# Performance work log

Measured on AMD Instinct MI355X. Metric: run time of the kernel, lower is better.

## Reference

```python
import jax, jax.numpy as jnp
import numpy as np

NC, NB, NT = 512, 128, 256   # feats dims: [channels, batch, time]
H = 512                      # hidden_size
NCLS = 97                    # num_classes
NUM_STEPS = 32               # fixed decode length (= text_length.max())


def setup_inputs() -> dict:
    key = jax.random.key(0)
    ks = jax.random.split(key, 12)
    s = 1.0 / np.sqrt(H)
    inp = {
        "feats": jax.random.normal(ks[0], (NC, NB, NT), jnp.float32),
        "text_length": jnp.full((NB,), NUM_STEPS, jnp.int32),
        # AttentionCell params
        "Wi2h": jax.random.normal(ks[1], (H, NC), jnp.float32) * s,   # i2h, no bias
        "Wh2h": jax.random.normal(ks[2], (H, H), jnp.float32) * s,
        "bh2h": jax.random.normal(ks[3], (H,), jnp.float32) * s,
        "Wscore": jax.random.normal(ks[4], (1, H), jnp.float32) * s,  # score, no bias
        # GRUCell params (gate order: r, z, n as in PyTorch)
        "Wih": jax.random.normal(ks[5], (3 * H, NC), jnp.float32) * s,
        "Whh": jax.random.normal(ks[6], (3 * H, H), jnp.float32) * s,
        "bih": jax.random.normal(ks[7], (3 * H,), jnp.float32) * s,
        "bhh": jax.random.normal(ks[8], (3 * H,), jnp.float32) * s,
        # generator: Linear(hidden_size, num_classes - 1)
        "Wgen": jax.random.normal(ks[9], (NCLS - 1, H), jnp.float32) * s,
        "bgen": jax.random.normal(ks[10], (NCLS - 1,), jnp.float32) * s,
    }
    return inp


def reference(feats, text_length, Wi2h, Wh2h, bh2h, Wscore, Wih, Whh, bih, bhh, Wgen, bgen):
    # feats: [nC, nB, nT]
    nC, nB, nT = feats.shape
    # i2h(feats) is step-independent -> hoist out of the loop (same math)
    feats_proj = jnp.einsum('cbt,hc->bth', feats, Wi2h)  # [nB, nT, H]
    w_score = Wscore[0]                                   # [H]

    def step(h, _):
        # additive attention
        hp = h @ Wh2h.T + bh2h                                  # [nB, H]
        e = jnp.tanh(feats_proj + hp[:, None, :]) @ w_score     # [nB, nT]
        alpha = jax.nn.softmax(e, axis=1)                       # [nB, nT]
        context = jnp.einsum('cbt,bt->bc', feats, alpha)        # [nB, nC]
        # GRUCell(context, h), PyTorch semantics
        gi = context @ Wih.T + bih                              # [nB, 3H]
        gh = h @ Whh.T + bhh                                    # [nB, 3H]
        ir, iz, in_ = jnp.split(gi, 3, axis=1)
        hr, hz, hn = jnp.split(gh, 3, axis=1)
        r = jax.nn.sigmoid(ir + hr)
        z = jax.nn.sigmoid(iz + hz)
        n = jnp.tanh(in_ + r * hn)
        h_new = (1.0 - z) * n + z * h
        return h_new, h_new

    h0 = jnp.zeros((nB, feats_proj.shape[-1]), feats.dtype)
    _, hiddens = jax.lax.scan(step, h0, None, length=NUM_STEPS)  # [T, nB, H]
    # all lengths == NUM_STEPS -> gather is a per-batch flatten
    new_hiddens = hiddens.transpose(1, 0, 2).reshape(-1, hiddens.shape[-1])  # [nB*T, H]
    probs = new_hiddens @ Wgen.T + bgen                          # [nB*T, NCLS-1]
    return probs
```

## Files before the change

kernel.cpp:

```cpp
#include <hip/hip_runtime.h>
#include <math.h>

#define NBATCH 128
#define NTIME  256
#define NCH    512
#define NH     512
#define NSTEPS 32
#define NOUT   96
#define MTOT   32768

typedef __attribute__((ext_vector_type(8))) short short8v;
typedef __attribute__((ext_vector_type(4))) float f32x4;

__device__ __forceinline__ float fast_tanh(float x) {
    x = fminf(fmaxf(x, -30.f), 30.f);
    float u = __expf(2.f * x);
    return (u - 1.f) / (u + 1.f);
}
__device__ __forceinline__ float fast_sigmoid(float x) {
    x = fminf(fmaxf(x, -30.f), 30.f);
    return 1.f / (1.f + __expf(-x));
}
__device__ __forceinline__ float wave_reduce_sum(float s) {
    #pragma unroll
    for (int off = 32; off; off >>= 1) s += __shfl_xor(s, off, 64);
    return s;
}
__device__ __forceinline__ float wave_reduce_max(float s) {
    #pragma unroll
    for (int off = 32; off; off >>= 1) s = fmaxf(s, __shfl_xor(s, off, 64));
    return s;
}
__device__ __forceinline__ unsigned short f2bf(float f) {
    unsigned u = __builtin_bit_cast(unsigned, f);
    return (unsigned short)((u + 0x7FFFu + ((u >> 16) & 1u)) >> 16);
}
__device__ __forceinline__ float bflo(unsigned u) {
    return __builtin_bit_cast(float, u << 16);
}
__device__ __forceinline__ float bfhi(unsigned u) {
    return __builtin_bit_cast(float, u & 0xFFFF0000u);
}

__global__ __launch_bounds__(256) void k_w2bf(const float* __restrict__ W,
                                              unsigned short* __restrict__ Wb) {
    #pragma unroll
    for (int r = 0; r < 4; ++r) {
        int idx = (blockIdx.x * 256 + threadIdx.x) + r * 16384;
        float4 v = *(const float4*)(W + (size_t)idx * 4);
        ushort4 o;
        o.x = f2bf(v.x); o.y = f2bf(v.y); o.z = f2bf(v.z); o.w = f2bf(v.w);
        *(ushort4*)(Wb + (size_t)idx * 4) = o;
    }
}

__global__ __launch_bounds__(256) void k_feats2bf(const float* __restrict__ feats,
                                                  unsigned short* __restrict__ Fb) {
    __shared__ float tl[64][65];
    const int m0 = (blockIdx.x & 511) * 64;
    const int k0 = (blockIdx.x >> 9) * 64;
    const int tid = threadIdx.x;
    #pragma unroll
    for (int p = 0; p < 4; ++p) {
        int fid = tid + p * 256;
        int row = fid >> 4, c4 = fid & 15;
        float4 v = *(const float4*)(feats + (size_t)(k0 + row) * MTOT + m0 + c4 * 4);
        tl[row][c4 * 4 + 0] = v.x; tl[row][c4 * 4 + 1] = v.y;
        tl[row][c4 * 4 + 2] = v.z; tl[row][c4 * 4 + 3] = v.w;
    }
    __syncthreads();
    #pragma unroll
    for (int p = 0; p < 4; ++p) {
        int cid = tid + p * 256;
        int mm = cid >> 4, ch = cid & 15;
        ushort4 o;
        o.x = f2bf(tl[ch * 4 + 0][mm]);
        o.y = f2bf(tl[ch * 4 + 1][mm]);
        o.z = f2bf(tl[ch * 4 + 2][mm]);
        o.w = f2bf(tl[ch * 4 + 3][mm]);
        *(ushort4*)(Fb + (size_t)(m0 + mm) * 512 + k0 + ch * 4) = o;
    }
}

__global__ __launch_bounds__(1024) void k_fcopy(const float* __restrict__ f,
                                                unsigned short* __restrict__ o) {
    int gid = blockIdx.x * 1024 + threadIdx.x;
    float4 v = *(const float4*)(f + (size_t)gid * 4);
    ushort4 s;
    s.x = f2bf(v.x); s.y = f2bf(v.y); s.z = f2bf(v.z); s.w = f2bf(v.w);
    *(ushort4*)(o + (size_t)gid * 4) = s;
}

__global__ __launch_bounds__(256) void k_fp_mfma(const unsigned short* __restrict__ Wb,
                                                 const unsigned short* __restrict__ Fb,
                                                 unsigned short* __restrict__ fp_bf) {
    __shared__ char SB[49152];
    unsigned short* As = (unsigned short*)SB;
    unsigned short* Bs = (unsigned short*)(SB + 16384);
    float* tl = (float*)SB;
    const int m0 = (blockIdx.x & 127) * 256;
    const int h0 = (blockIdx.x >> 7) * 128;
    const int tid = threadIdx.x;
    const int lane = tid & 63, wid = tid >> 6;
    const int wh = wid & 1, wm = wid >> 1;
    f32x4 acc[4][8];
    #pragma unroll
    for (int i = 0; i < 4; ++i)
        #pragma unroll
        for (int j = 0; j < 8; ++j) acc[i][j] = (f32x4)0.f;

    for (int k0 = 0; k0 < 512; k0 += 64) {
        #pragma unroll
        for (int i = 0; i < 4; ++i) {
            int cid = tid + i * 256;
            int row = cid >> 3, ch = cid & 7;
            uint4 v = *(const uint4*)(Wb + (size_t)(h0 + row) * 512 + k0 + ch * 8);
            *(uint4*)(As + row * 64 + ((ch ^ (row & 7)) << 3)) = v;
        }
        #pragma unroll
        for (int i = 0; i < 8; ++i) {
            int cid = tid + i * 256;
            int row = cid >> 3, ch = cid & 7;
            uint4 v = *(const uint4*)(Fb + (size_t)(m0 + row) * 512 + k0 + ch * 8);
            *(uint4*)(Bs + row * 64 + ((ch ^ (row & 7)) << 3)) = v;
        }
        __syncthreads();
        #pragma unroll
        for (int ks = 0; ks < 2; ++ks) {
            short8v a[4], b[8];
            #pragma unroll
            for (int hf = 0; hf < 4; ++hf) {
                int row = wh * 64 + hf * 16 + (lane & 15);
                int ch = ks * 4 + (lane >> 4);
                a[hf] = *(const short8v*)(As + row * 64 + ((ch ^ (row & 7)) << 3));
            }
            #pragma unroll
            for (int mf = 0; mf < 8; ++mf) {
                int row = wm * 128 + mf * 16 + (lane & 15);
                int ch = ks * 4 + (lane >> 4);
                b[mf] = *(const short8v*)(Bs + row * 64 + ((ch ^ (row & 7)) << 3));
            }
            #pragma unroll
            for (int hf = 0; hf < 4; ++hf)
                #pragma unroll
                for (int mf = 0; mf < 8; ++mf)
                    acc[hf][mf] = __builtin_amdgcn_mfma_f32_16x16x32_bf16(
                        a[hf], b[mf], acc[hf][mf], 0, 0, 0);
        }
        __syncthreads();
    }
    #pragma unroll
    for (int hf = 0; hf < 4; ++hf) {
        #pragma unroll
        for (int mf = 0; mf < 8; ++mf) {
            int ml = wm * 128 + mf * 16 + (lane & 15);
            int col = wh * 16 + (lane >> 4) * 4;
            tl[ml * 33 + col + 0] = acc[hf][mf][0];
            tl[ml * 33 + col + 1] = acc[hf][mf][1];
            tl[ml * 33 + col + 2] = acc[hf][mf][2];
            tl[ml * 33 + col + 3] = acc[hf][mf][3];
        }
        __syncthreads();
        #pragma unroll
        for (int mi = 0; mi < 8; ++mi) {
            int ml = (tid >> 3) + mi * 32;
            int hl4 = (tid & 7) * 4;
            float v0 = tl[ml * 33 + hl4 + 0];
            float v1 = tl[ml * 33 + hl4 + 1];
            float v2 = tl[ml * 33 + hl4 + 2];
            float v3 = tl[ml * 33 + hl4 + 3];
            int hg = h0 + ((hl4 < 16) ? (hf * 16 + hl4) : (64 + hf * 16 + hl4 - 16));
            ushort4 o;
            o.x = f2bf(v0); o.y = f2bf(v1); o.z = f2bf(v2); o.w = f2bf(v3);
            *(ushort4*)(fp_bf + (size_t)(m0 + ml) * 512 + hg) = o;
        }
        __syncthreads();
    }
}

__global__ __launch_bounds__(256) void k_wt(const float* __restrict__ W,
                                            float* __restrict__ WT) {
    __shared__ float tl[32][33];
    const int bi = blockIdx.x & 15, bj = blockIdx.x >> 4;
    const int tx = threadIdx.x & 31, ty8 = threadIdx.x >> 5;
    #pragma unroll
    for (int i = 0; i < 4; ++i) {
        int r = ty8 * 4 + i;
        tl[r][tx] = W[(size_t)(bj * 32 + r) * NH + bi * 32 + tx];
    }
    __syncthreads();
    #pragma unroll
    for (int i = 0; i < 4; ++i) {
        int c = ty8 * 4 + i;
        WT[(size_t)(bi * 32 + c) * NH + bj * 32 + tx] = tl[tx][c];
    }
}

__global__ __launch_bounds__(1024) void k_hp0(const float* __restrict__ bh2h,
                                              float* __restrict__ hp) {
    int i = blockIdx.x * 1024 + threadIdx.x;
    hp[i] = bh2h[i & 511];
}

__global__ __launch_bounds__(512) void k_e(const unsigned short* __restrict__ fp_bf,
                                           const float* __restrict__ hp,
                                           const float* __restrict__ wscore,
                                           float* __restrict__ e) {
    const int b = blockIdx.x >> 2;
    const int t0 = (blockIdx.x & 3) * 64;
    const int tid = threadIdx.x;
    const int lane = tid & 63, w = tid >> 6;
    float4 h0 = *(const float4*)(hp + (size_t)b * NH + lane * 8);
    float4 h1 = *(const float4*)(hp + (size_t)b * NH + lane * 8 + 4);
    float4 w0 = *(const float4*)(wscore + lane * 8);
    float4 w1 = *(const float4*)(wscore + lane * 8 + 4);
    #pragma unroll 2
    for (int it = 0; it < 8; ++it) {
        int t = t0 + w * 8 + it;
        uint4 v = *(const uint4*)(fp_bf + (size_t)(b * NTIME + t) * NH + lane * 8);
        float s = fast_tanh(bflo(v.x) + h0.x) * w0.x + fast_tanh(bfhi(v.x) + h0.y) * w0.y +
                  fast_tanh(bflo(v.y) + h0.z) * w0.z + fast_tanh(bfhi(v.y) + h0.w) * w0.w +
                  fast_tanh(bflo(v.z) + h1.x) * w1.x + fast_tanh(bfhi(v.z) + h1.y) * w1.y +
                  fast_tanh(bflo(v.w) + h1.z) * w1.z + fast_tanh(bfhi(v.w) + h1.w) * w1.w;
        s = wave_reduce_sum(s);
        if (lane == 0) e[b * NTIME + t] = s;
    }
}

__global__ __launch_bounds__(512) void k_ctx2(const float* __restrict__ e,
                                              const unsigned short* __restrict__ featsb,
                                              float* __restrict__ ctx) {
    __shared__ float als[256];
    __shared__ float red[8];
    const int b = blockIdx.x >> 2;
    const int c0 = (blockIdx.x & 3) * 128;
    const int tid = threadIdx.x;
    const int lane = tid & 63, w = tid >> 6;
    float v = (tid < 256) ? e[b * NTIME + tid] : -3.4e38f;
    float m = wave_reduce_max(v);
    if (lane == 0) red[w] = m;
    __syncthreads();
    m = red[0];
    #pragma unroll
    for (int i = 1; i < 8; ++i) m = fmaxf(m, red[i]);
    float ex = (tid < 256) ? __expf(v - m) : 0.f;
    float s = wave_reduce_sum(ex);
    __syncthreads();
    if (lane == 0) red[w] = s;
    __syncthreads();
    s = 0.f;
    #pragma unroll
    for (int i = 0; i < 8; ++i) s += red[i];
    if (tid < 256) als[tid] = ex / s;
    __syncthreads();

    float4 al = *(const float4*)&als[lane * 4];
    #pragma unroll 4
    for (int cc = 0; cc < 16; ++cc) {
        int c = c0 + w * 16 + cc;
        uint2 fv = *(const uint2*)(featsb + (size_t)(c * NBATCH + b) * NTIME + lane * 4);
        float sc = bflo(fv.x) * al.x + bfhi(fv.x) * al.y +
                   bflo(fv.y) * al.z + bfhi(fv.y) * al.w;
        sc = wave_reduce_sum(sc);
        if (lane == 0) ctx[(size_t)b * NCH + c] = sc;
    }
}

__global__ __launch_bounds__(1024) void k_gates(const float* __restrict__ ctx,
                                                const float* __restrict__ h,
                                                const float* __restrict__ Wih,
                                                const float* __restrict__ Whh,
                                                float* __restrict__ g2) {
    __shared__ float S[16384 + 8192];
    float* A_ldsT = S;
    float* scr    = S + 16384;
    const int blk = blockIdx.x;
    const int g   = blk >> 5;
    const int j0  = (blk & 31) * 16;
    const float* A = (g < 3) ? ctx : h;
    const float* W = (g < 3) ? Wih : Whh;
    const int tid = threadIdx.x;
    const int m2  = tid & 63;
    const int q   = __builtin_amdgcn_readfirstlane(tid >> 6);
    const int nq  = q & 3, kq = q >> 2;
    const float* Wr0 = W + (size_t)((g % 3) * 512 + j0 + nq * 4 + 0) * NH;
    const float* Wr1 = W + (size_t)((g % 3) * 512 + j0 + nq * 4 + 1) * NH;
    const float* Wr2 = W + (size_t)((g % 3) * 512 + j0 + nq * 4 + 2) * NH;
    const float* Wr3 = W + (size_t)((g % 3) * 512 + j0 + nq * 4 + 3) * NH;
    float acc[2][4] = {};
    for (int kt = 0; kt < 4; ++kt) {
        {
            int m = tid & 127, kc = tid >> 7;
            #pragma unroll
            for (int q4 = 0; q4 < 4; ++q4) {
                int kk = kc * 16 + q4 * 4;
                float4 vv = *(const float4*)(A + (size_t)m * NH + kt * 128 + kk);
                A_ldsT[(kk + 0) * 128 + m] = vv.x;
                A_ldsT[(kk + 1) * 128 + m] = vv.y;
                A_ldsT[(kk + 2) * 128 + m] = vv.z;
                A_ldsT[(kk + 3) * 128 + m] = vv.w;
            }
        }
        __syncthreads();
        const int kbase = kt * 128;
        #pragma unroll 8
        for (int kk = kq * 32; kk < kq * 32 + 32; ++kk) {
            float a0 = A_ldsT[kk * 128 + m2];
            float a1 = A_ldsT[kk * 128 + m2 + 64];
            float w0 = Wr0[kbase + kk], w1 = Wr1[kbase + kk];
            float w2 = Wr2[kbase + kk], w3 = Wr3[kbase + kk];
            acc[0][0] += a0 * w0; acc[0][1] += a0 * w1;
            acc[0][2] += a0 * w2; acc[0][3] += a0 * w3;
            acc[1][0] += a1 * w0; acc[1][1] += a1 * w1;
            acc[1][2] += a1 * w2; acc[1][3] += a1 * w3;
        }
        __syncthreads();
    }
    #pragma unroll
    for (int hi = 0; hi < 2; ++hi)
        #pragma unroll
        for (int r = 0; r < 4; ++r)
            scr[(kq * 16 + nq * 4 + r) * 128 + m2 + 64 * hi] = acc[hi][r];
    __syncthreads();
    #pragma unroll
    for (int rep = 0; rep < 2; ++rep) {
        int oid = tid + rep * 1024;
        int m = oid & 127, nl = oid >> 7;
        float vv = scr[(0 * 16 + nl) * 128 + m] + scr[(1 * 16 + nl) * 128 + m] +
                   scr[(2 * 16 + nl) * 128 + m] + scr[(3 * 16 + nl) * 128 + m];
        g2[(size_t)(g * 512 + j0 + nl) * NBATCH + m] = vv;
    }
}

__global__ __launch_bounds__(1024) void k_comb_hp(const float* __restrict__ g2,
                                                  const float* __restrict__ hprev,
                                                  float* __restrict__ hidn,
                                                  const float* __restrict__ bih,
                                                  const float* __restrict__ bhh,
                                                  const float* __restrict__ WT,
                                                  const float* __restrict__ bh2h,
                                                  float* __restrict__ hp) {
    __shared__ float h_s[4 * 512];
    __shared__ float scr2[16 * 4 * 16 * 4];
    const int blk = blockIdx.x;
    const int b0 = (blk >> 3) * 4;
    const int jbase = (blk & 7) * 64;
    const int tid = threadIdx.x;
    #pragma unroll
    for (int rep = 0; rep < 2; ++rep) {
        int idx = tid + rep * 1024;
        int bi = idx & 3, kk = idx >> 2;
        int b = b0 + bi;
        float ir = g2[(size_t)(0 * 512 + kk) * NBATCH + b] + bih[kk];
        float iz = g2[(size_t)(1 * 512 + kk) * NBATCH + b] + bih[512 + kk];
        float in_ = g2[(size_t)(2 * 512 + kk) * NBATCH + b] + bih[1024 + kk];
        float hr = g2[(size_t)(3 * 512 + kk) * NBATCH + b] + bhh[kk];
        float hz = g2[(size_t)(4 * 512 + kk) * NBATCH + b] + bhh[512 + kk];
        float hn = g2[(size_t)(5 * 512 + kk) * NBATCH + b] + bhh[1024 + kk];
        float r = fast_sigmoid(ir + hr);
        float z = fast_sigmoid(iz + hz);
        float ng = fast_tanh(in_ + r * hn);
        float hv = hprev[(size_t)b * NH + kk];
        float hnew = (1.f - z) * ng + z * hv;
        h_s[bi * 512 + kk] = hnew;
        if ((blk & 7) == 0) hidn[(size_t)b * NH + kk] = hnew;
    }
    __syncthreads();
    {
        const int jq = tid & 15, bi = (tid >> 4) & 3, kq = tid >> 6;
        const int j = jbase + jq * 4;
        float4 acc = make_float4(0.f, 0.f, 0.f, 0.f);
        #pragma unroll 8
        for (int kk = 0; kk < 32; ++kk) {
            int k = kq * 32 + kk;
            float4 wv = *(const float4*)(WT + (size_t)k * NH + j);
            float hv = h_s[bi * 512 + k];
            acc.x += hv * wv.x; acc.y += hv * wv.y;
            acc.z += hv * wv.z; acc.w += hv * wv.w;
        }
        *(float4*)&scr2[((kq * 4 + bi) * 16 + jq) * 4] = acc;
    }
    __syncthreads();
    if (tid < 64) {
        const int bi = tid >> 4, jq = tid & 15;
        float4 sum = make_float4(0.f, 0.f, 0.f, 0.f);
        #pragma unroll
        for (int kq = 0; kq < 16; ++kq) {
            float4 p = *(const float4*)&scr2[((kq * 4 + bi) * 16 + jq) * 4];
            sum.x += p.x; sum.y += p.y; sum.z += p.z; sum.w += p.w;
        }
        int j = jbase + jq * 4;
        float4 bb = *(const float4*)(bh2h + j);
        sum.x += bb.x; sum.y += bb.y; sum.z += bb.z; sum.w += bb.w;
        *(float4*)(hp + (size_t)(b0 + bi) * NH + j) = sum;
    }
}

__global__ __launch_bounds__(256) void k_gen(const float* __restrict__ hid,
                                             const float* __restrict__ Wgen,
                                             const float* __restrict__ bgen,
                                             float* __restrict__ out) {
    __shared__ float As[32][36];
    __shared__ float Bs[32][97];
    const int m0 = blockIdx.x * 32;
    const int tid = threadIdx.x;
    const int tx = tid & 31, ty = tid >> 5;
    float acc[4][3] = {};
    for (int k0 = 0; k0 < 512; k0 += 32) {
        {
            int mm = tid >> 3, kq = (tid & 7) << 2;
            int m = m0 + mm, s = m & 31, b = m >> 5;
            float4 v = *(const float4*)(hid + (size_t)(s + 1) * 65536 + b * 512 + k0 + kq);
            *(float4*)(&As[mm][kq]) = v;
        }
        #pragma unroll
        for (int i = 0; i < 3; ++i) {
            int f4 = tid + i * 256;
            int nn = f4 >> 3, kq = (f4 & 7) << 2;
            float4 v = *(const float4*)(Wgen + (size_t)nn * 512 + k0 + kq);
            Bs[kq + 0][nn] = v.x; Bs[kq + 1][nn] = v.y;
            Bs[kq + 2][nn] = v.z; Bs[kq + 3][nn] = v.w;
        }
        __syncthreads();
        #pragma unroll
        for (int kk = 0; kk < 32; ++kk) {
            float bv[3];
            #pragma unroll
            for (int j = 0; j < 3; ++j) bv[j] = Bs[kk][tx * 3 + j];
            #pragma unroll
            for (int i = 0; i < 4; ++i) {
                float a = As[ty * 4 + i][kk];
                #pragma unroll
                for (int j = 0; j < 3; ++j) acc[i][j] += a * bv[j];
            }
        }
        __syncthreads();
    }
    #pragma unroll
    for (int i = 0; i < 4; ++i)
        #pragma unroll
        for (int j = 0; j < 3; ++j)
            out[(size_t)(m0 + ty * 4 + i) * NOUT + tx * 3 + j] = acc[i][j] + bgen[tx * 3 + j];
}

extern "C" void kernel_launch(void* const* d_in, const int* in_sizes, int n_in,
                              void* d_out, int out_size, void* d_ws, size_t ws_size,
                              hipStream_t stream) {
    const float* feats  = (const float*)d_in[0];
    const float* Wi2h   = (const float*)d_in[2];
    const float* Wh2h   = (const float*)d_in[3];
    const float* bh2h   = (const float*)d_in[4];
    const float* Wscore = (const float*)d_in[5];
    const float* Wih    = (const float*)d_in[6];
    const float* Whh    = (const float*)d_in[7];
    const float* bih    = (const float*)d_in[8];
    const float* bhh    = (const float*)d_in[9];
    const float* Wgen   = (const float*)d_in[10];
    const float* bgen   = (const float*)d_in[11];
    float* out = (float*)d_out;

    float* ws  = (float*)d_ws;
    unsigned short* fp_bf = (unsigned short*)ws;
    float* hid   = ws + 8388608;
    float* WT    = hid + 2162688;
    float* hpctx = WT + 262144;
    unsigned short* Wb     = (unsigned short*)(hpctx + 65536);
    unsigned short* Fb     = (unsigned short*)(hpctx + 65536 + 131072);
    unsigned short* featsb = Fb;

    float* e  = out;
    float* g2 = out;

    hipMemsetAsync(hid, 0, 65536 * sizeof(float), stream);
    k_wt<<<256, 256, 0, stream>>>(Wh2h, WT);
    k_w2bf<<<64, 256, 0, stream>>>(Wi2h, Wb);
    k_feats2bf<<<4096, 256, 0, stream>>>(feats, Fb);
    k_fp_mfma<<<512, 256, 0, stream>>>(Wb, Fb, fp_bf);
    k_fcopy<<<4096, 1024, 0, stream>>>(feats, featsb);
    k_hp0<<<64, 1024, 0, stream>>>(bh2h, hpctx);

    for (int s = 0; s < NSTEPS; ++s) {
        const float* h = hid + (size_t)s * 65536;
        float* hn      = hid + (size_t)(s + 1) * 65536;
        k_e<<<512, 512, 0, stream>>>(fp_bf, hpctx, Wscore, e);
        k_ctx2<<<512, 512, 0, stream>>>(e, featsb, hpctx);
        k_gates<<<192, 1024, 0, stream>>>(hpctx, h, Wih, Whh, g2);
        k_comb_hp<<<256, 1024, 0, stream>>>(g2, h, hn, bih, bhh, WT, bh2h, hpctx);
    }
    k_gen<<<128, 256, 0, stream>>>(hid, Wgen, bgen, out);
}
```

Baseline: 1.852 ms.

## Replace fp32 GRU gate GEMM with bf16 MFMA kernel and bf16 weights

Pre-converts Wih/Whh to bf16 and computes the per-step GRU gate projections with a bf16 MFMA tiled GEMM (24 blocks of 128x128), consuming bf16 context and a bf16 copy of h. Also stores the transposed Wh2h in bf16 for the hp projection in the combine kernel. This aims to cut the scalar fp32 FMA cost and weight bandwidth of the gate GEMM each step, at the cost of bf16 rounding of inputs and weights and low grid occupancy.

```diff
diff --git a/kernel.cpp b/kernel.cpp
--- a/kernel.cpp
+++ b/kernel.cpp
@@ -51,6 +51,21 @@
         ushort4 o;
         o.x = f2bf(v.x); o.y = f2bf(v.y); o.z = f2bf(v.z); o.w = f2bf(v.w);
         *(ushort4*)(Wb + (size_t)idx * 4) = o;
+    }
+}
+
+__global__ __launch_bounds__(256) void k_wg2bf(const float* __restrict__ Wih,
+                                               const float* __restrict__ Whh,
+                                               unsigned short* __restrict__ Wgb) {
+    #pragma unroll
+    for (int r = 0; r < 4; ++r) {
+        int idx = (blockIdx.x * 256 + threadIdx.x) + r * 98304;
+        const float* src = (idx < 196608) ? (Wih + (size_t)idx * 4)
+                                          : (Whh + (size_t)(idx - 196608) * 4);
+        float4 v = *(const float4*)src;
+        ushort4 o;
+        o.x = f2bf(v.x); o.y = f2bf(v.y); o.z = f2bf(v.z); o.w = f2bf(v.w);
+        *(ushort4*)(Wgb + (size_t)idx * 4) = o;
     }
 }
 
@@ -179,7 +194,7 @@
 }
 
 __global__ __launch_bounds__(256) void k_wt(const float* __restrict__ W,
-                                            float* __restrict__ WT) {
+                                            unsigned short* __restrict__ WTb) {
     __shared__ float tl[32][33];
     const int bi = blockIdx.x & 15, bj = blockIdx.x >> 4;
     const int tx = threadIdx.x & 31, ty8 = threadIdx.x >> 5;
@@ -192,7 +207,7 @@
     #pragma unroll
     for (int i = 0; i < 4; ++i) {
         int c = ty8 * 4 + i;
-        WT[(size_t)(bi * 32 + c) * NH + bj * 32 + tx] = tl[tx][c];
+        WTb[(size_t)(bi * 32 + c) * NH + bj * 32 + tx] = f2bf(tl[tx][c]);
     }
 }
 
@@ -229,7 +244,7 @@
 
 __global__ __launch_bounds__(512) void k_ctx2(const float* __restrict__ e,
                                               const unsigned short* __restrict__ featsb,
-                                              float* __restrict__ ctx) {
+                                              unsigned short* __restrict__ ctx_bf) {
     __shared__ float als[256];
     __shared__ float red[8];
     const int b = blockIdx.x >> 2;
@@ -262,82 +277,76 @@
         float sc = bflo(fv.x) * al.x + bfhi(fv.x) * al.y +
                    bflo(fv.y) * al.z + bfhi(fv.y) * al.w;
         sc = wave_reduce_sum(sc);
-        if (lane == 0) ctx[(size_t)b * NCH + c] = sc;
-    }
-}
-
-__global__ __launch_bounds__(1024) void k_gates(const float* __restrict__ ctx,
-                                                const float* __restrict__ h,
-                                                const float* __restrict__ Wih,
-                                                const float* __restrict__ Whh,
-                                                float* __restrict__ g2) {
-    __shared__ float S[16384 + 8192];
-    float* A_ldsT = S;
-    float* scr    = S + 16384;
-    const int blk = blockIdx.x;
-    const int g   = blk >> 5;
-    const int j0  = (blk & 31) * 16;
-    const float* A = (g < 3) ? ctx : h;
-    const float* W = (g < 3) ? Wih : Whh;
-    const int tid = threadIdx.x;
-    const int m2  = tid & 63;
-    const int q   = __builtin_amdgcn_readfirstlane(tid >> 6);
-    const int nq  = q & 3, kq = q >> 2;
-    const float* Wr0 = W + (size_t)((g % 3) * 512 + j0 + nq * 4 + 0) * NH;
-    const float* Wr1 = W + (size_t)((g % 3) * 512 + j0 + nq * 4 + 1) * NH;
-    const float* Wr2 = W + (size_t)((g % 3) * 512 + j0 + nq * 4 + 2) * NH;
-    const float* Wr3 = W + (size_t)((g % 3) * 512 + j0 + nq * 4 + 3) * NH;
-    float acc[2][4] = {};
-    for (int kt = 0; kt < 4; ++kt) {
-        {
-            int m = tid & 127, kc = tid >> 7;
-            #pragma unroll
-            for (int q4 = 0; q4 < 4; ++q4) {
-                int kk = kc * 16 + q4 * 4;
-                float4 vv = *(const float4*)(A + (size_t)m * NH + kt * 128 + kk);
-                A_ldsT[(kk + 0) * 128 + m] = vv.x;
-                A_ldsT[(kk + 1) * 128 + m] = vv.y;
-                A_ldsT[(kk + 2) * 128 + m] = vv.z;
-                A_ldsT[(kk + 3) * 128 + m] = vv.w;
+        if (lane == 0) ctx_bf[(size_t)b * NCH + c] = f2bf(sc);
+    }
+}
+
+__global__ __launch_bounds__(256) void k_gmfma(const unsigned short* __restrict__ ctx_bf,
+                                               const unsigned short* __restrict__ h_bf,
+                                               const unsigned short* __restrict__ Wgb,
+                                               float* __restrict__ g2) {
+    __shared__ unsigned short As[128 * 64];
+    __shared__ unsigned short Bs[128 * 64];
+    const int j0 = blockIdx.x * 128;
+    const unsigned short* A = (j0 < 1536) ? ctx_bf : h_bf;
+    const int tid = threadIdx.x;
+    const int lane = tid & 63, wid = tid >> 6;
+    const int wb = wid & 1, wj = wid >> 1;
+    f32x4 acc[4][4];
+    #pragma unroll
+    for (int i = 0; i < 4; ++i)
+        #pragma unroll
+        for (int j = 0; j < 4; ++j) acc[i][j] = (f32x4)0.f;
+
+    for (int k0 = 0; k0 < 512; k0 += 64) {
+        #pragma unroll
+        for (int i = 0; i < 4; ++i) {
+            int cid = tid + i * 256;
+            int row = cid >> 3, ch = cid & 7;
+            uint4 va = *(const uint4*)(A + (size_t)row * 512 + k0 + ch * 8);
+            *(uint4*)(As + row * 64 + ((ch ^ (row & 7)) << 3)) = va;
+            uint4 vb = *(const uint4*)(Wgb + (size_t)(j0 + row) * 512 + k0 + ch * 8);
+            *(uint4*)(Bs + row * 64 + ((ch ^ (row & 7)) << 3)) = vb;
+        }
+        __syncthreads();
+        #pragma unroll
+        for (int ks = 0; ks < 2; ++ks) {
+            short8v a[4], b[4];
+            #pragma unroll
+            for (int f = 0; f < 4; ++f) {
+                int rowa = wb * 64 + f * 16 + (lane & 15);
+                int rowb = wj * 64 + f * 16 + (lane & 15);
+                int ch = ks * 4 + (lane >> 4);
+                a[f] = *(const short8v*)(As + rowa * 64 + ((ch ^ (rowa & 7)) << 3));
+                b[f] = *(const short8v*)(Bs + rowb * 64 + ((ch ^ (rowb & 7)) << 3));
             }
-        }
-        __syncthreads();
-        const int kbase = kt * 128;
-        #pragma unroll 8
-        for (int kk = kq * 32; kk < kq * 32 + 32; ++kk) {
-            float a0 = A_ldsT[kk * 128 + m2];
-            float a1 = A_ldsT[kk * 128 + m2 + 64];
-            float w0 = Wr0[kbase + kk], w1 = Wr1[kbase + kk];
-            float w2 = Wr2[kbase + kk], w3 = Wr3[kbase + kk];
-            acc[0][0] += a0 * w0; acc[0][1] += a0 * w1;
-            acc[0][2] += a0 * w2; acc[0][3] += a0 * w3;
-            acc[1][0] += a1 * w0; acc[1][1] += a1 * w1;
-            acc[1][2] += a1 * w2; acc[1][3] += a1 * w3;
-        }
-        __syncthreads();
-    }
-    #pragma unroll
-    for (int hi = 0; hi < 2; ++hi)
-        #pragma unroll
-        for (int r = 0; r < 4; ++r)
-            scr[(kq * 16 + nq * 4 + r) * 128 + m2 + 64 * hi] = acc[hi][r];
-    __syncthreads();
-    #pragma unroll
-    for (int rep = 0; rep < 2; ++rep) {
-        int oid = tid + rep * 1024;
-        int m = oid & 127, nl = oid >> 7;
-        float vv = scr[(0 * 16 + nl) * 128 + m] + scr[(1 * 16 + nl) * 128 + m] +
-                   scr[(2 * 16 + nl) * 128 + m] + scr[(3 * 16 + nl) * 128 + m];
-        g2[(size_t)(g * 512 + j0 + nl) * NBATCH + m] = vv;
+            #pragma unroll
+            for (int bf = 0; bf < 4; ++bf)
+                #pragma unroll
+                for (int jf = 0; jf < 4; ++jf)
+                    acc[bf][jf] = __builtin_amdgcn_mfma_f32_16x16x32_bf16(
+                        a[bf], b[jf], acc[bf][jf], 0, 0, 0);
+        }
+        __syncthreads();
+    }
+    #pragma unroll
+    for (int bf = 0; bf < 4; ++bf) {
+        int b = wb * 64 + bf * 16 + (lane >> 4) * 4;
+        #pragma unroll
+        for (int jf = 0; jf < 4; ++jf) {
+            int j = j0 + wj * 64 + jf * 16 + (lane & 15);
+            *(f32x4*)(g2 + (size_t)j * NBATCH + b) = acc[bf][jf];
+        }
     }
 }
 
 __global__ __launch_bounds__(1024) void k_comb_hp(const float* __restrict__ g2,
                                                   const float* __restrict__ hprev,
                                                   float* __restrict__ hidn,
+                                                  unsigned short* __restrict__ h_bf,
                                                   const float* __restrict__ bih,
                                                   const float* __restrict__ bhh,
-                                                  const float* __restrict__ WT,
+                                                  const unsigned short* __restrict__ WTb,
                                                   const float* __restrict__ bh2h,
                                                   float* __restrict__ hp) {
     __shared__ float h_s[4 * 512];
@@ -351,19 +360,22 @@
         int idx = tid + rep * 1024;
         int bi = idx & 3, kk = idx >> 2;
         int b = b0 + bi;
-        float ir = g2[(size_t)(0 * 512 + kk) * NBATCH + b] + bih[kk];
-        float iz = g2[(size_t)(1 * 512 + kk) * NBATCH + b] + bih[512 + kk];
+        float ir  = g2[(size_t)(0 * 512 + kk) * NBATCH + b] + bih[kk];
+        float iz  = g2[(size_t)(1 * 512 + kk) * NBATCH + b] + bih[512 + kk];
         float in_ = g2[(size_t)(2 * 512 + kk) * NBATCH + b] + bih[1024 + kk];
-        float hr = g2[(size_t)(3 * 512 + kk) * NBATCH + b] + bhh[kk];
-        float hz = g2[(size_t)(4 * 512 + kk) * NBATCH + b] + bhh[512 + kk];
-        float hn = g2[(size_t)(5 * 512 + kk) * NBATCH + b] + bhh[1024 + kk];
+        float hr  = g2[(size_t)(3 * 512 + kk) * NBATCH + b] + bhh[kk];
+        float hz  = g2[(size_t)(4 * 512 + kk) * NBATCH + b] + bhh[512 + kk];
+        float hn  = g2[(size_t)(5 * 512 + kk) * NBATCH + b] + bhh[1024 + kk];
         float r = fast_sigmoid(ir + hr);
         float z = fast_sigmoid(iz + hz);
         float ng = fast_tanh(in_ + r * hn);
         float hv = hprev[(size_t)b * NH + kk];
         float hnew = (1.f - z) * ng + z * hv;
         h_s[bi * 512 + kk] = hnew;
-        if ((blk & 7) == 0) hidn[(size_t)b * NH + kk] = hnew;
+        if ((blk & 7) == 0) {
+            hidn[(size_t)b * NH + kk] = hnew;
+            h_bf[(size_t)b * NH + kk] = f2bf(hnew);
+        }
     }
     __syncthreads();
     {
@@ -373,10 +385,10 @@
         #pragma unroll 8
         for (int kk = 0; kk < 32; ++kk) {
             int k = kq * 32 + kk;
-            float4 wv = *(const float4*)(WT + (size_t)k * NH + j);
+            uint2 wq = *(const uint2*)(WTb + (size_t)k * NH + j);
             float hv = h_s[bi * 512 + k];
-            acc.x += hv * wv.x; acc.y += hv * wv.y;
-            acc.z += hv * wv.z; acc.w += hv * wv.w;
+            acc.x += hv * bflo(wq.x); acc.y += hv * bfhi(wq.x);
+            acc.z += hv * bflo(wq.y); acc.w += hv * bfhi(wq.y);
         }
         *(float4*)&scr2[((kq * 4 + bi) * 16 + jq) * 4] = acc;
     }
@@ -460,20 +472,25 @@
     float* out = (float*)d_out;
 
     float* ws  = (float*)d_ws;
-    unsigned short* fp_bf = (unsigned short*)ws;
-    float* hid   = ws + 8388608;
-    float* WT    = hid + 2162688;
-    float* hpctx = WT + 262144;
-    unsigned short* Wb     = (unsigned short*)(hpctx + 65536);
-    unsigned short* Fb     = (unsigned short*)(hpctx + 65536 + 131072);
+    unsigned short* fp_bf  = (unsigned short*)ws;
+    float*          hid    = ws + 8388608;
+    float*          hpctx  = hid + 2162688;
+    unsigned short* ctx_bf = (unsigned short*)(hpctx + 65536);
+    unsigned short* h_bf   = (unsigned short*)(hpctx + 65536 + 32768);
+    unsigned short* WTb    = (unsigned short*)(hpctx + 65536 + 65536);
+    unsigned short* Wgb    = (unsigned short*)(hpctx + 65536 + 65536 + 131072);
+    unsigned short* Wb     = (unsigned short*)(hpctx + 65536 + 65536 + 131072 + 786432);
+    unsigned short* Fb     = (unsigned short*)(hpctx + 65536 + 65536 + 131072 + 786432 + 131072);
     unsigned short* featsb = Fb;
 
     float* e  = out;
     float* g2 = out;
 
     hipMemsetAsync(hid, 0, 65536 * sizeof(float), stream);
-    k_wt<<<256, 256, 0, stream>>>(Wh2h, WT);
+    hipMemsetAsync(h_bf, 0, 65536 * sizeof(unsigned short), stream);
+    k_wt<<<256, 256, 0, stream>>>(Wh2h, WTb);
     k_w2bf<<<64, 256, 0, stream>>>(Wi2h, Wb);
+    k_wg2bf<<<384, 256, 0, stream>>>(Wih, Whh, Wgb);
     k_feats2bf<<<4096, 256, 0, stream>>>(feats, Fb);
     k_fp_mfma<<<512, 256, 0, stream>>>(Wb, Fb, fp_bf);
     k_fcopy<<<4096, 1024, 0, stream>>>(feats, featsb);
@@ -483,9 +500,9 @@
         const float* h = hid + (size_t)s * 65536;
         float* hn      = hid + (size_t)(s + 1) * 65536;
         k_e<<<512, 512, 0, stream>>>(fp_bf, hpctx, Wscore, e);
-        k_ctx2<<<512, 512, 0, stream>>>(e, featsb, hpctx);
-        k_gates<<<192, 1024, 0, stream>>>(hpctx, h, Wih, Whh, g2);
-        k_comb_hp<<<256, 1024, 0, stream>>>(g2, h, hn, bih, bhh, WT, bh2h, hpctx);
+        k_ctx2<<<512, 512, 0, stream>>>(e, featsb, ctx_bf);
+        k_gmfma<<<24, 256, 0, stream>>>(ctx_bf, h_bf, Wgb, g2);
+        k_comb_hp<<<256, 1024, 0, stream>>>(g2, h, hn, h_bf, bih, bhh, WTb, bh2h, hpctx);
     }
     k_gen<<<128, 256, 0, stream>>>(hid, Wgen, bgen, out);
 }
```

Result: faster. 1.665 ms (-10.1%).
